# Kernel optimization log

Hardware: AMD Instinct MI355X
Metric: run time of the kernel (lower is better)

Reference implementation:

```python
import jax, jax.numpy as jnp
import numpy as np

NHEAD = 8
TOPKS = (8, 8)  # topk per level, coarse -> fine


def _to_bshd(x):
    # [B, C, H, W] -> [B, H*W, nhead, d]  (matches rearrange 'b c h w -> b (h w) c' + view)
    b, c, h, w = x.shape
    return jnp.transpose(x.reshape(b, c, h * w), (0, 2, 1)).reshape(b, h * w, NHEAD, c // NHEAD)


def _coarse_level(q, k, v, topk):
    b, c, h, w = k.shape
    d = c // NHEAD
    q_, k_, v_ = _to_bshd(q), _to_bshd(k), _to_bshd(v)
    temp = 1.0 / (d ** 0.5)
    A = jax.nn.softmax(jnp.einsum('nlhd,nshd->nlsh', q_, k_) * temp, axis=2)  # [b,L,S,h]
    _, idx = jax.lax.top_k(jnp.swapaxes(A, 2, 3), topk)  # [b,L,h,k]
    idx = jnp.swapaxes(idx, 2, 3)                        # [b,L,k,h]
    msg = jnp.einsum('nlsh,nshd->nlhd', A, v_)           # [b,L,h,d]
    topk_pos = jnp.stack([idx // w, idx % w])            # [2,b,L,k,h]
    return msg, topk_pos


def _fine_level(q, k, v, topk_pos, topk_prev, topk):
    b, c, h0, w0 = q.shape
    w1 = k.shape[3]
    d = c // NHEAD
    k_, v_ = _to_bshd(k), _to_bshd(v)
    H2, W2 = h0 // 2, w0 // 2
    L0 = H2 * W2
    # query grouped into 2x2 quads: [b, L0, 4, h, d]
    q_ = q.reshape(b, c, H2, 2, W2, 2).transpose(0, 2, 4, 3, 5, 1).reshape(b, L0, 4, NHEAD, d)
    tp = topk_pos * 2  # coarse positions -> fine grid
    cand = [(tp[0] + x) * w1 + tp[1] + y for x in (0, 1) for y in (0, 1)]
    t2 = topk_prev * 4
    idx = jnp.stack(cand, axis=3).reshape(b, L0, t2, NHEAD)  # [b,L,t2,h]
    idx_bh = idx.transpose(0, 3, 1, 2).reshape(b, NHEAD, L0 * t2)

    def gather(p):  # p: [b,S,h,d] -> gathered [b,L,t2,h,d]
        g = jnp.take_along_axis(jnp.swapaxes(p, 1, 2), idx_bh[..., None], axis=2)
        return g.reshape(b, NHEAD, L0, t2, d).transpose(0, 2, 3, 1, 4)

    tk, tv = gather(k_), gather(v_)
    temp = 1.0 / (d ** 0.5)
    A = jax.nn.softmax(jnp.einsum('blqhd,blthd->blqth', q_, tk) * temp, axis=3)  # [b,L,4,t2,h]
    _, ti = jax.lax.top_k(jnp.moveaxis(A, 3, 4), topk)  # [b,L,4,h,k]
    ti = jnp.moveaxis(ti, 4, 3)                         # [b,L,4,k,h]
    msg = jnp.einsum('blqth,blthd->blqhd', A, tv)       # [b,L,4,h,d]
    idx_b = jnp.broadcast_to(idx[:, :, None], (b, L0, 4, t2, NHEAD))
    gidx = jnp.take_along_axis(idx_b, ti, axis=3)       # [b,L,4,k,h] flat fine-grid indices
    gidx = gidx.reshape(b, H2, W2, 2, 2, topk, NHEAD).transpose(0, 1, 3, 2, 4, 5, 6)
    gidx = gidx.reshape(b, h0 * w0, topk, NHEAD)
    return msg, gidx


def _forward(q_fine, q_coarse, k_fine, k_coarse, v_fine, v_coarse, weight):
    msg0, topk_pos = _coarse_level(q_coarse, k_coarse, v_coarse, TOPKS[0])
    msg1, _ = _fine_level(q_fine, k_fine, v_fine, topk_pos, TOPKS[0], TOPKS[1])
    w = jax.nn.softmax(weight, axis=0)
    fm = msg0 * w[0]                  # [b,Lc,h,d]
    fm = fm[:, :, None] + msg1 * w[1]  # [b,Lc,4,h,d]
    b, Hc, Wc = q_coarse.shape[0], q_coarse.shape[2], q_coarse.shape[3]
    d = fm.shape[-1]
    # rearrange 'b (H W) (t1 t2) h d -> b (H t1 W t2) h d'
    fm = fm.reshape(b, Hc, Wc, 2, 2, NHEAD, d).transpose(0, 1, 3, 2, 4, 5, 6)
    return fm.reshape(b, Hc * Wc * 4, NHEAD, d)


def setup_inputs() -> dict:
    key = jax.random.key(0)
    ks = jax.random.split(key, 7)
    B, C = 4, 128
    return {
        'q_fine': jax.random.normal(ks[0], (B, C, 64, 64), jnp.float32),
        'q_coarse': jax.random.normal(ks[1], (B, C, 32, 32), jnp.float32),
        'k_fine': jax.random.normal(ks[2], (B, C, 64, 64), jnp.float32),
        'k_coarse': jax.random.normal(ks[3], (B, C, 32, 32), jnp.float32),
        'v_fine': jax.random.normal(ks[4], (B, C, 64, 64), jnp.float32),
        'v_coarse': jax.random.normal(ks[5], (B, C, 32, 32), jnp.float32),
        'weight': jax.random.normal(ks[6], (2,), jnp.float32),
    }


def reference(q_fine, q_coarse, k_fine, k_coarse, v_fine, v_coarse, weight):
    return _forward(q_fine, q_coarse, k_fine, k_coarse, v_fine, v_coarse, weight)
```

## Files before the change

kernel.cpp:

```cpp
#include <hip/hip_runtime.h>
#include <stdint.h>

#define TEMP 0.25f

typedef unsigned short u16;
typedef short v8s __attribute__((ext_vector_type(8)));
typedef float v4f __attribute__((ext_vector_type(4)));

static __device__ __forceinline__ uint32_t f2b_bits(float f){
    union { float f; uint32_t i; } x; x.f = f;
    uint32_t u = x.i;
    return (u + 0x7FFFu + ((u >> 16) & 1u)) >> 16;
}
static __device__ __forceinline__ float b2f(u16 u){
    union { uint32_t i; float f; } x; x.i = ((uint32_t)u) << 16; return x.f;
}
static __device__ __forceinline__ float bl(uint32_t u){
    union { uint32_t i; float f; } x; x.i = u << 16; return x.f;
}
static __device__ __forceinline__ float bh(uint32_t u){
    union { uint32_t i; float f; } x; x.i = u & 0xffff0000u; return x.f;
}
static __device__ __forceinline__ uint4 pack8(const uint32_t* e){
    return make_uint4(e[0] | (e[1] << 16), e[2] | (e[3] << 16),
                      e[4] | (e[5] << 16), e[6] | (e[7] << 16));
}
static __device__ __forceinline__ uint32_t split2_pk(float x){
    float hi = __uint_as_float(__float_as_uint(x) & 0xffff0000u);
    float lo = x - hi;
    uint32_t pk;
    asm("v_cvt_pk_bf16_f32 %0, %1, %2" : "=v"(pk) : "v"(hi), "v"(lo));
    return pk;
}
union U8S { uint4 u; v8s s; };
union I4S { int i[4]; v8s s; };
static __device__ __forceinline__ v8s asv8s(uint4 u){ U8S x; x.u = u; return x.s; }

template<int C>
static __device__ __forceinline__ float dppf(float x){
    int xi = __float_as_int(x);
    return __int_as_float(__builtin_amdgcn_update_dpp(xi, xi, C, 0xf, 0xf, false));
}
static __device__ __forceinline__ float red16_max(float m){
    m = fmaxf(m, dppf<0xB1>(m));  m = fmaxf(m, dppf<0x4E>(m));
    m = fmaxf(m, dppf<0x141>(m)); m = fmaxf(m, dppf<0x140>(m));
    return m;
}
static __device__ __forceinline__ float red16_sum(float s){
    s += dppf<0xB1>(s);  s += dppf<0x4E>(s);
    s += dppf<0x141>(s); s += dppf<0x140>(s);
    return s;
}
static __device__ __forceinline__ float sw16(float x){
    return __int_as_float(__builtin_amdgcn_ds_swizzle(__float_as_int(x), 0x401F));
}
template<int C>
static __device__ __forceinline__ uint64_t dppmax64(uint64_t k){
    int hi = (int)(uint32_t)(k >> 32), lo = (int)(uint32_t)k;
    uint32_t oh = (uint32_t)__builtin_amdgcn_update_dpp(hi, hi, C, 0xf, 0xf, false);
    uint32_t ol = (uint32_t)__builtin_amdgcn_update_dpp(lo, lo, C, 0xf, 0xf, false);
    uint64_t ok = ((uint64_t)oh << 32) | ol;
    return ok > k ? ok : k;
}
static __device__ __forceinline__ uint64_t red16_maxkey(uint64_t k){
    k = dppmax64<0xB1>(k);  k = dppmax64<0x4E>(k);
    k = dppmax64<0x141>(k); k = dppmax64<0x140>(k);
    return k;
}

__global__ __launch_bounds__(256)
void pack_coarse(const float* __restrict__ kc, const float* __restrict__ vc,
                 uint4* __restrict__ KP1, uint4* __restrict__ KP3,
                 uint4* __restrict__ VP1)
{
    const int bh = blockIdx.x;
    const int kv = blockIdx.y;
    const int z  = blockIdx.z;
    const int b = bh >> 3, h = bh & 7;
    const int tid = threadIdx.x;
    const size_t sbase = (size_t)(b * 128 + h * 16) * 1024;
    const size_t fbase = (size_t)bh * 64 * 64;

    #pragma unroll
    for (int it = 0; it < 2; ++it){
        int task = it * 256 + tid;
        int kt = z * 8 + (task >> 6), ln = task & 63;
        int quad = ln >> 4, col = ln & 15;
        if (kv == 0){
            uint32_t e1[8], e3[8];
            #pragma unroll
            for (int j = 0; j < 8; ++j){
                int dch = (quad & 1) * 8 + j;
                float x = kc[sbase + (size_t)dch * 1024 + kt * 16 + col];
                uint32_t u0 = f2b_bits(x);
                float r1 = x - b2f((u16)u0);
                uint32_t u1 = f2b_bits(r1);
                float r2 = r1 - b2f((u16)u1);
                uint32_t u2 = f2b_bits(r2);
                e1[j] = (quad < 2) ? u0 : u1;
                e3[j] = (quad < 2) ? u2 : u0;
            }
            KP1[fbase + kt * 64 + ln] = pack8(e1);
            KP3[fbase + kt * 64 + ln] = pack8(e3);
        } else {
            uint32_t e[8];
            #pragma unroll
            for (int j = 0; j < 8; ++j){
                int key = kt * 16 + (quad & 1) * 8 + j;
                float x = vc[sbase + (size_t)col * 1024 + key];
                uint32_t u0 = f2b_bits(x);
                uint32_t u1 = f2b_bits(x - b2f((u16)u0));
                e[j] = (quad < 2) ? u0 : u1;
            }
            VP1[fbase + kt * 64 + ln] = pack8(e);
        }
    }
}

__global__ __launch_bounds__(256)
void pack_all(const float* __restrict__ kf, const float* __restrict__ vf,
              const float* __restrict__ qf,
              const float* __restrict__ kc, const float* __restrict__ vc,
              uint32_t* __restrict__ packed, float* __restrict__ qT,
              uint4* __restrict__ KP1, uint4* __restrict__ KP3,
              uint4* __restrict__ VP1)
{
    __shared__ float tile[64][129];
    const int bid = blockIdx.x;
    const int tid = threadIdx.x;

    if (bid < 768){
        const int pt = bid & 63, b = (bid >> 6) & 3, z = bid >> 8;
        const float* src = (z == 0) ? kf : (z == 1) ? vf : qf;
        const int pos0 = pt * 64;

        #pragma unroll
        for (int it = 0; it < 8; ++it){
            int task = it * 256 + tid;
            int ch = task >> 4, p4 = task & 15;
            float4 v = *(const float4*)(src + (size_t)(b * 128 + ch) * 4096 + pos0 + p4 * 4);
            tile[p4*4+0][ch] = v.x; tile[p4*4+1][ch] = v.y;
            tile[p4*4+2][ch] = v.z; tile[p4*4+3][ch] = v.w;
        }
        __syncthreads();

        if (z == 2){
            #pragma unroll
            for (int it = 0; it < 8; ++it){
                int task = it * 256 + tid;
                int p = task >> 5, c4 = task & 31;
                float4 v = make_float4(tile[p][c4*4+0], tile[p][c4*4+1],
                                       tile[p][c4*4+2], tile[p][c4*4+3]);
                *(float4*)(qT + ((size_t)(b * 4096) + pos0 + p) * 128 + c4 * 4) = v;
            }
        } else {
            const int x = pt;
            #pragma unroll
            for (int it = 0; it < 2; ++it){
                int task = it * 256 + tid;
                int hq = task >> 6, y = task & 63;
                int pprime = ((x >> 1) * 32 + (y >> 1)) * 4 + (x & 1) * 2 + (y & 1);
                size_t line = (size_t)(b * 8 + hq) * 4096 + pprime;
                uint32_t dw[8];
                #pragma unroll
                for (int i = 0; i < 8; ++i){
                    uint32_t lo = f2b_bits(tile[y][hq * 16 + 2 * i]);
                    uint32_t hi = f2b_bits(tile[y][hq * 16 + 2 * i + 1]);
                    dw[i] = lo | (hi << 16);
                }
                uint4* dst4 = (uint4*)packed + line * 4 + z * 2;
                dst4[0] = make_uint4(dw[0], dw[1], dw[2], dw[3]);
                dst4[1] = make_uint4(dw[4], dw[5], dw[6], dw[7]);
            }
        }
    } else {
        const int f2 = bid - 768;
        const int bh = f2 & 31, kv = (f2 >> 5) & 1, z = f2 >> 6;
        const int b = bh >> 3, h = bh & 7;
        const size_t sbase = (size_t)(b * 128 + h * 16) * 1024;
        const size_t fbase = (size_t)bh * 64 * 64;

        #pragma unroll
        for (int it = 0; it < 2; ++it){
            int task = it * 256 + tid;
            int kt = z * 8 + (task >> 6), ln = task & 63;
            int quad = ln >> 4, col = ln & 15;
            if (kv == 0){
                uint32_t e1[8], e3[8];
                #pragma unroll
                for (int j = 0; j < 8; ++j){
                    int dch = (quad & 1) * 8 + j;
                    float x = kc[sbase + (size_t)dch * 1024 + kt * 16 + col];
                    uint32_t u0 = f2b_bits(x);
                    float r1 = x - b2f((u16)u0);
                    uint32_t u1 = f2b_bits(r1);
                    float r2 = r1 - b2f((u16)u1);
                    uint32_t u2 = f2b_bits(r2);
                    e1[j] = (quad < 2) ? u0 : u1;
                    e3[j] = (quad < 2) ? u2 : u0;
                }
                KP1[fbase + kt * 64 + ln] = pack8(e1);
                KP3[fbase + kt * 64 + ln] = pack8(e3);
            } else {
                uint32_t e[8];
                #pragma unroll
                for (int j = 0; j < 8; ++j){
                    int key = kt * 16 + (quad & 1) * 8 + j;
                    float x = vc[sbase + (size_t)col * 1024 + key];
                    uint32_t pk = split2_pk(x);
                    e[j] = (quad < 2) ? (pk & 0xffffu) : (pk >> 16);
                }
                VP1[fbase + kt * 64 + ln] = pack8(e);
            }
        }
    }
}

__global__ __launch_bounds__(256)
void coarse_mfma(const float* __restrict__ qc,
                 const uint4* __restrict__ KP1, const uint4* __restrict__ KP3,
                 const uint4* __restrict__ VP1,
                 float* __restrict__ msg0, int* __restrict__ topk_out)
{
    const int ltile = blockIdx.x;
    const int h = blockIdx.y, b = blockIdx.z;
    const int bh = b * 8 + h;
    const int tid = threadIdx.x, lane = tid & 63, wv = tid >> 6;
    const int quad = lane >> 4, col = lane & 15;
    const int lanex = lane ^ 32;
    const int lbase = ltile * 16;

    __shared__ uint32_t tls[4][2 * 320];
    __shared__ float rred[2][4][16];
    __shared__ float pvred[4][16][16];
    __shared__ float tkv[4][16][8];
    __shared__ int   tki[4][16][8];

    v8s a1, a3;
    {
        int row = lbase + col;
        int dch0 = (quad & 1) * 8;
        #pragma unroll
        for (int j = 0; j < 8; ++j){
            float x = qc[(size_t)(b * 128 + h * 16 + dch0 + j) * 1024 + row] * TEMP;
            uint32_t u0 = f2b_bits(x);
            float r1 = x - b2f((u16)u0);
            uint32_t u1 = f2b_bits(r1);
            float r2 = r1 - b2f((u16)u1);
            uint32_t u2 = f2b_bits(r2);
            a1[j] = (short)(quad < 2 ? u0 : u1);
            a3[j] = (short)(quad < 2 ? u0 : u2);
        }
    }

    const size_t fbase = (size_t)bh * 64 * 64;
    v4f sc[16];
    #pragma unroll
    for (int kt = 0; kt < 16; ++kt){
        int ktg = wv * 16 + kt;
        v8s b1 = asv8s(KP1[fbase + (size_t)ktg * 64 + lane]);
        v8s b2 = asv8s(KP1[fbase + (size_t)ktg * 64 + lanex]);
        v8s b3 = asv8s(KP3[fbase + (size_t)ktg * 64 + lane]);
        v4f c = {0.f, 0.f, 0.f, 0.f};
        c = __builtin_amdgcn_mfma_f32_16x16x32_bf16(a1, b1, c, 0, 0, 0);
        c = __builtin_amdgcn_mfma_f32_16x16x32_bf16(a1, b2, c, 0, 0, 0);
        c = __builtin_amdgcn_mfma_f32_16x16x32_bf16(a3, b3, c, 0, 0, 0);
        sc[kt] = c;
    }

    #pragma unroll
    for (int r = 0; r < 4; ++r){
        float m = sc[0][r];
        #pragma unroll
        for (int kt = 1; kt < 16; ++kt) m = fmaxf(m, sc[kt][r]);
        m = red16_max(m);
        if (col == 0) rred[0][wv][quad * 4 + r] = m;
    }
    __syncthreads();
    #pragma unroll
    for (int r = 0; r < 4; ++r){
        int row = quad * 4 + r;
        float m = fmaxf(fmaxf(rred[0][0][row], rred[0][1][row]),
                        fmaxf(rred[0][2][row], rred[0][3][row]));
        #pragma unroll
        for (int kt = 0; kt < 16; ++kt) sc[kt][r] = __expf(sc[kt][r] - m);
    }
    #pragma unroll
    for (int r = 0; r < 4; ++r){
        float s = 0.f;
        #pragma unroll
        for (int kt = 0; kt < 16; ++kt) s += sc[kt][r];
        s = red16_sum(s);
        if (col == 0) rred[1][wv][quad * 4 + r] = s;
    }

    v4f acc = {0.f, 0.f, 0.f, 0.f};
    uint32_t* tw = tls[wv];
    const int rdbase = col * 20 + 8 * (quad & 1);
    const uint32_t selp = (quad < 2) ? 0x05040100u : 0x07060302u;
    #pragma unroll
    for (int kb = 0; kb < 8; ++kb){
        #pragma unroll
        for (int ki = 0; ki < 2; ++ki){
            int kt = kb * 2 + ki;
            #pragma unroll
            for (int r = 0; r < 4; ++r)
                tw[ki * 320 + (quad * 4 + r) * 20 + col] = split2_pk(sc[kt][r]);
        }
        __builtin_amdgcn_s_waitcnt(0xC07F);
        #pragma unroll
        for (int ki = 0; ki < 2; ++ki){
            int kt = kb * 2 + ki;
            uint4 d0 = *(const uint4*)&tw[ki * 320 + rdbase];
            uint4 d1 = *(const uint4*)&tw[ki * 320 + rdbase + 4];
            I4S ux;
            ux.i[0] = __builtin_amdgcn_perm(d0.y, d0.x, selp);
            ux.i[1] = __builtin_amdgcn_perm(d0.w, d0.z, selp);
            ux.i[2] = __builtin_amdgcn_perm(d1.y, d1.x, selp);
            ux.i[3] = __builtin_amdgcn_perm(d1.w, d1.z, selp);
            v8s ap = ux.s;
            v8s bv1 = asv8s(VP1[fbase + (size_t)(wv * 16 + kt) * 64 + lane]);
            v8s bv2 = asv8s(VP1[fbase + (size_t)(wv * 16 + kt) * 64 + lanex]);
            acc = __builtin_amdgcn_mfma_f32_16x16x32_bf16(ap, bv1, acc, 0, 0, 0);
            acc = __builtin_amdgcn_mfma_f32_16x16x32_bf16(ap, bv2, acc, 0, 0, 0);
        }
    }
    #pragma unroll
    for (int r = 0; r < 4; ++r) pvred[wv][quad * 4 + r][col] = acc[r];

    #pragma unroll
    for (int r = 0; r < 4; ++r){
        int row = quad * 4 + r;
        float wval = 0.f; int widx = 0;
        #pragma unroll
        for (int rnd = 0; rnd < 8; ++rnd){
            float bv = sc[0][r]; int bk = 0;
            #pragma unroll
            for (int kt = 1; kt < 16; ++kt){
                bool g = sc[kt][r] > bv;
                bv = g ? sc[kt][r] : bv; bk = g ? kt : bk;
            }
            int bi = bk * 16 + col;
            uint64_t k = ((uint64_t)(uint32_t)__float_as_int(bv) << 32)
                       | (uint32_t)(~bi);
            k = red16_maxkey(k);
            bv = __int_as_float((int)(uint32_t)(k >> 32));
            bi = (int)(~(uint32_t)k);
            if ((bi & 15) == col){
                int ktw = bi >> 4;
                #pragma unroll
                for (int kt = 0; kt < 16; ++kt)
                    if (kt == ktw) sc[kt][r] = -1.0f;
            }
            if (col == rnd){ wval = bv; widx = wv * 256 + bi; }
        }
        if (col < 8){ tkv[wv][row][col] = wval; tki[wv][row][col] = widx; }
    }
    __syncthreads();

    {
        int row = tid >> 4, dd = tid & 15;
        float v = pvred[0][row][dd] + pvred[1][row][dd] +
                  pvred[2][row][dd] + pvred[3][row][dd];
        float s = rred[1][0][row] + rred[1][1][row] +
                  rred[1][2][row] + rred[1][3][row];
        msg0[((size_t)((b * 1024 + lbase + row) * 8 + h)) * 16 + dd] = v / s;
    }
    if (tid < 16){
        int row = tid;
        int* tp = topk_out + (((b * 1024 + lbase + row) * 8 + h) * 8);
        int p[4] = {0, 0, 0, 0};
        #pragma unroll
        for (int rnd = 0; rnd < 8; ++rnd){
            float bv = -3.0f; int bw = 0, bi = 0x7fffffff;
            #pragma unroll
            for (int w = 0; w < 4; ++w){
                float v = tkv[w][row][p[w]];
                int   i = tki[w][row][p[w]];
                bool g = (v > bv) || (v == bv && i < bi);
                bv = g ? v : bv; bi = g ? i : bi; bw = g ? w : bw;
            }
            tp[rnd] = bi;
            p[bw]++;
        }
    }
}

__global__ __launch_bounds__(512, 2)
void coarse_kernel(const float* __restrict__ qc, const float* __restrict__ kc,
                   const float* __restrict__ vc, float* __restrict__ msg0,
                   int* __restrict__ topk_out)
{
    const int ltile = blockIdx.x;
    const int h = blockIdx.y, b = blockIdx.z;
    const int tid = threadIdx.x;
    const int lane = tid & 63, wv = tid >> 6;
    const int lbase = ltile * 32;
    __shared__ float sKV[16 * 1024];
    const size_t base = (size_t)(b * 128 + h * 16) * 1024;
    {
        const float4* gK = (const float4*)(kc + base);
        float4* lK = (float4*)sKV;
        #pragma unroll
        for (int i = 0; i < 8; ++i) lK[tid + 512 * i] = gK[tid + 512 * i];
    }
    float qreg[4];
    {
        int dq = lane & 15;
        #pragma unroll
        for (int li = 0; li < 4; ++li){
            int l = lbase + wv * 4 + li;
            qreg[li] = qc[base + (size_t)dq * 1024 + l] * TEMP;
        }
    }
    __syncthreads();
    float p[4][16];
    #pragma unroll
    for (int li = 0; li < 4; ++li)
        #pragma unroll
        for (int j = 0; j < 16; ++j) p[li][j] = 0.f;
    #pragma unroll
    for (int dch = 0; dch < 16; ++dch){
        float kf[16];
        #pragma unroll
        for (int ch = 0; ch < 4; ++ch){
            float4 kv = *(const float4*)&sKV[dch * 1024 + ch * 256 + (lane << 2)];
            kf[ch*4+0] = kv.x; kf[ch*4+1] = kv.y; kf[ch*4+2] = kv.z; kf[ch*4+3] = kv.w;
        }
        float qs[4];
        #pragma unroll
        for (int li = 0; li < 4; ++li) qs[li] = __shfl(qreg[li], dch);
        #pragma unroll
        for (int li = 0; li < 4; ++li)
            #pragma unroll
            for (int j = 0; j < 16; ++j) p[li][j] = fmaf(qs[li], kf[j], p[li][j]);
    }
    float invs[4];
    #pragma unroll
    for (int li = 0; li < 4; ++li){
        float m = p[li][0];
        #pragma unroll
        for (int j = 1; j < 16; ++j) m = fmaxf(m, p[li][j]);
        #pragma unroll
        for (int off = 32; off > 0; off >>= 1) m = fmaxf(m, __shfl_xor(m, off));
        float s = 0.f;
        #pragma unroll
        for (int j = 0; j < 16; ++j){ p[li][j] = __expf(p[li][j] - m); s += p[li][j]; }
        #pragma unroll
        for (int off = 32; off > 0; off >>= 1) s += __shfl_xor(s, off);
        invs[li] = 1.0f / s;
    }
    __syncthreads();
    {
        const float4* gV = (const float4*)(vc + base);
        float4* lV = (float4*)sKV;
        #pragma unroll
        for (int i = 0; i < 8; ++i) lV[tid + 512 * i] = gV[tid + 512 * i];
    }
    __syncthreads();
    float outv = 0.f;
    #pragma unroll
    for (int dd = 0; dd < 16; ++dd){
        float vf[16];
        #pragma unroll
        for (int ch = 0; ch < 4; ++ch){
            float4 vv = *(const float4*)&sKV[dd * 1024 + ch * 256 + (lane << 2)];
            vf[ch*4+0] = vv.x; vf[ch*4+1] = vv.y; vf[ch*4+2] = vv.z; vf[ch*4+3] = vv.w;
        }
        float a[4];
        #pragma unroll
        for (int li = 0; li < 4; ++li){
            float s = 0.f;
            #pragma unroll
            for (int j = 0; j < 16; ++j) s = fmaf(p[li][j], vf[j], s);
            a[li] = s;
        }
        #pragma unroll
        for (int off = 32; off > 0; off >>= 1)
            #pragma unroll
            for (int li = 0; li < 4; ++li) a[li] += __shfl_xor(a[li], off);
        #pragma unroll
        for (int li = 0; li < 4; ++li)
            outv = (lane == li * 16 + dd) ? a[li] * invs[li] : outv;
    }
    {
        int li = lane >> 4, dd = lane & 15;
        int l = lbase + wv * 4 + li;
        msg0[(size_t)((b * 1024 + l) * 8 + h) * 16 + dd] = outv;
    }
    const int lanebase = lane << 4;
    int mytk = 0;
    for (int r = 0; r < 8; ++r){
        float bv[4]; int bi[4];
        #pragma unroll
        for (int li = 0; li < 4; ++li){
            float v0[8]; int j0[8];
            #pragma unroll
            for (int k = 0; k < 8; ++k){
                bool g = p[li][2*k+1] > p[li][2*k];
                v0[k] = g ? p[li][2*k+1] : p[li][2*k];
                j0[k] = g ? 2*k+1 : 2*k;
            }
            float v1[4]; int j1[4];
            #pragma unroll
            for (int k = 0; k < 4; ++k){
                bool g = v0[2*k+1] > v0[2*k];
                v1[k] = g ? v0[2*k+1] : v0[2*k];
                j1[k] = g ? j0[2*k+1] : j0[2*k];
            }
            float v2[2]; int j2[2];
            #pragma unroll
            for (int k = 0; k < 2; ++k){
                bool g = v1[2*k+1] > v1[2*k];
                v2[k] = g ? v1[2*k+1] : v1[2*k];
                j2[k] = g ? j1[2*k+1] : j1[2*k];
            }
            bool g3 = v2[1] > v2[0];
            bv[li] = g3 ? v2[1] : v2[0];
            bi[li] = lanebase | (g3 ? j2[1] : j2[0]);
        }
        #pragma unroll
        for (int off = 32; off > 0; off >>= 1){
            #pragma unroll
            for (int li = 0; li < 4; ++li){
                float ov = __shfl_xor(bv[li], off);
                int   oi = __shfl_xor(bi[li], off);
                bool g = (ov > bv[li]) || (ov == bv[li] && oi < bi[li]);
                bv[li] = g ? ov : bv[li];
                bi[li] = g ? oi : bi[li];
            }
        }
        #pragma unroll
        for (int li = 0; li < 4; ++li){
            #pragma unroll
            for (int j = 0; j < 16; ++j)
                p[li][j] = (bi[li] == (lanebase | j)) ? -1.0f : p[li][j];
            mytk = (lane == li * 8 + r) ? bi[li] : mytk;
        }
    }
    if (lane < 32){
        int li = lane >> 3, r = lane & 7;
        int jw = mytk & 15, lw = mytk >> 4;
        int s = ((jw >> 2) << 8) | (lw << 2) | (jw & 3);
        int l = lbase + wv * 4 + li;
        topk_out[((b * 1024 + l) * 8 + h) * 8 + r] = s;
    }
}

__global__ __launch_bounds__(256)
void pack_kernel(const float* __restrict__ kf, const float* __restrict__ vf,
                 const float* __restrict__ qf,
                 uint32_t* __restrict__ packed, float* __restrict__ qT)
{
    const int pt = blockIdx.x;
    const int b  = blockIdx.y;
    const int z  = blockIdx.z;
    const float* src = (z == 0) ? kf : (z == 1) ? vf : qf;
    const int tid = threadIdx.x;
    __shared__ float tile[64][129];
    const int pos0 = pt * 64;

    #pragma unroll
    for (int it = 0; it < 8; ++it){
        int task = it * 256 + tid;
        int ch = task >> 4, p4 = task & 15;
        float4 v = *(const float4*)(src + (size_t)(b * 128 + ch) * 4096 + pos0 + p4 * 4);
        tile[p4*4+0][ch] = v.x; tile[p4*4+1][ch] = v.y;
        tile[p4*4+2][ch] = v.z; tile[p4*4+3][ch] = v.w;
    }
    __syncthreads();

    if (z == 2){
        #pragma unroll
        for (int it = 0; it < 8; ++it){
            int task = it * 256 + tid;
            int p = task >> 5, c4 = task & 31;
            float4 v = make_float4(tile[p][c4*4+0], tile[p][c4*4+1],
                                   tile[p][c4*4+2], tile[p][c4*4+3]);
            *(float4*)(qT + ((size_t)(b * 4096) + pos0 + p) * 128 + c4 * 4) = v;
        }
    } else {
        const int x = pt;
        #pragma unroll
        for (int it = 0; it < 2; ++it){
            int task = it * 256 + tid;
            int h = task >> 6, y = task & 63;
            int pprime = ((x >> 1) * 32 + (y >> 1)) * 4 + (x & 1) * 2 + (y & 1);
            size_t line = (size_t)(b * 8 + h) * 4096 + pprime;
            uint32_t dw[8];
            #pragma unroll
            for (int i = 0; i < 8; ++i){
                uint32_t lo = f2b_bits(tile[y][h * 16 + 2 * i]);
                uint32_t hi = f2b_bits(tile[y][h * 16 + 2 * i + 1]);
                dw[i] = lo | (hi << 16);
            }
            uint4* dst4 = (uint4*)packed + line * 4 + z * 2;
            dst4[0] = make_uint4(dw[0], dw[1], dw[2], dw[3]);
            dst4[1] = make_uint4(dw[4], dw[5], dw[6], dw[7]);
        }
    }
}

__global__ __launch_bounds__(256)
void fine_kernel(const float* __restrict__ qf, const float* __restrict__ kf,
                 const float* __restrict__ vf,
                 const float* __restrict__ qTg, const uint32_t* __restrict__ packed,
                 int transposed,
                 const float* __restrict__ wt,
                 const int* __restrict__ topk_in, const float* __restrict__ msg0,
                 float* __restrict__ out)
{
    const int l0 = blockIdx.x;
    const int b  = blockIdx.y;
    const int tid = threadIdx.x;

    __shared__ float vT[8][16][34];
    __shared__ float qT[8][4][16];
    __shared__ float pT[8][4][32];
    __shared__ int tkS[8][8];

    if (tid < 64) tkS[tid >> 3][tid & 7] =
        topk_in[((b * 1024 + l0) * 8 + (tid >> 3)) * 8 + (tid & 7)];
    __syncthreads();

    const int i = l0 >> 5, j = l0 & 31;
    const int hh = tid >> 5;
    const int t  = tid & 31;
    const int kk = t >> 2, cp = t & 3;

    float k[16];
    {
        int s = tkS[hh][kk];
        if (transposed){
            const uint4* pk = (const uint4*)packed;
            size_t line = (size_t)(b * 8 + hh) * 4096 + s * 4 + cp;
            uint4 a0 = pk[line*4+0], a1 = pk[line*4+1];
            uint4 a2 = pk[line*4+2], a3 = pk[line*4+3];
            k[0]=bl(a0.x);  k[1]=bh(a0.x);  k[2]=bl(a0.y);  k[3]=bh(a0.y);
            k[4]=bl(a0.z);  k[5]=bh(a0.z);  k[6]=bl(a0.w);  k[7]=bh(a0.w);
            k[8]=bl(a1.x);  k[9]=bh(a1.x);  k[10]=bl(a1.y); k[11]=bh(a1.y);
            k[12]=bl(a1.z); k[13]=bh(a1.z); k[14]=bl(a1.w); k[15]=bh(a1.w);
            vT[hh][0][t]=bl(a2.x);  vT[hh][1][t]=bh(a2.x);
            vT[hh][2][t]=bl(a2.y);  vT[hh][3][t]=bh(a2.y);
            vT[hh][4][t]=bl(a2.z);  vT[hh][5][t]=bh(a2.z);
            vT[hh][6][t]=bl(a2.w);  vT[hh][7][t]=bh(a2.w);
            vT[hh][8][t]=bl(a3.x);  vT[hh][9][t]=bh(a3.x);
            vT[hh][10][t]=bl(a3.y); vT[hh][11][t]=bh(a3.y);
            vT[hh][12][t]=bl(a3.z); vT[hh][13][t]=bh(a3.z);
            vT[hh][14][t]=bl(a3.w); vT[hh][15][t]=bh(a3.w);
        } else {
            int pos = (2 * (s >> 5) + (cp >> 1)) * 64 + 2 * (s & 31) + (cp & 1);
            size_t gb = (size_t)(b * 128 + hh * 16) * 4096 + pos;
            #pragma unroll
            for (int ch = 0; ch < 16; ++ch){
                k[ch] = kf[gb + (size_t)ch * 4096];
                vT[hh][ch][t] = vf[gb + (size_t)ch * 4096];
            }
        }
    }
    if (tid < 128){
        int qh = tid >> 4, aq = (tid >> 2) & 3, c4 = tid & 3;
        int qpos = (2 * i + (aq >> 1)) * 64 + 2 * j + (aq & 1);
        if (transposed){
            float4 u = *(const float4*)(qTg + ((size_t)(b * 4096) + qpos) * 128 + qh * 16 + c4 * 4);
            qT[qh][aq][c4*4+0] = u.x * TEMP;
            qT[qh][aq][c4*4+1] = u.y * TEMP;
            qT[qh][aq][c4*4+2] = u.z * TEMP;
            qT[qh][aq][c4*4+3] = u.w * TEMP;
        } else {
            #pragma unroll
            for (int c = 0; c < 4; ++c)
                qT[qh][aq][c4*4+c] =
                    qf[(size_t)(b * 128 + qh * 16 + c4 * 4 + c) * 4096 + qpos] * TEMP;
        }
    }
    __syncthreads();

    {
        float sc[4] = {0.f, 0.f, 0.f, 0.f};
        #pragma unroll
        for (int dch = 0; dch < 16; ++dch){
            float kv = k[dch];
            #pragma unroll
            for (int q = 0; q < 4; ++q) sc[q] = fmaf(qT[hh][q][dch], kv, sc[q]);
        }
        #pragma unroll
        for (int q = 0; q < 4; ++q){
            float m = red16_max(sc[q]);
            m = fmaxf(m, sw16(m));
            float e = __expf(sc[q] - m);
            float s = red16_sum(e);
            s += sw16(s);
            pT[hh][q][t] = e / s;
        }
    }
    __syncthreads();

    {
        float w0 = wt[0], w1 = wt[1];
        float mx = fmaxf(w0, w1);
        float e0 = __expf(w0 - mx), e1 = __expf(w1 - mx);
        float w0f = e0 / (e0 + e1), w1f = e1 / (e0 + e1);

        int q0 = (tid >> 4) & 1;
        int dd = tid & 15;
        float a0 = 0.f, a1 = 0.f;
        #pragma unroll
        for (int tt = 0; tt < 16; ++tt){
            float v0 = vT[hh][dd][tt * 2], v1 = vT[hh][dd][tt * 2 + 1];
            float2 pA = *(const float2*)&pT[hh][q0][tt * 2];
            float2 pB = *(const float2*)&pT[hh][q0 + 2][tt * 2];
            a0 = fmaf(pA.x, v0, a0); a0 = fmaf(pA.y, v1, a0);
            a1 = fmaf(pB.x, v0, a1); a1 = fmaf(pB.y, v1, a1);
        }
        float m0 = msg0[(size_t)((b * 1024 + l0) * 8 + hh) * 16 + dd];
        float o0 = w0f * m0 + w1f * a0;
        float o1 = w0f * m0 + w1f * a1;
        int posA = (2 * i) * 64 + 2 * j + q0;
        int posB = (2 * i + 1) * 64 + 2 * j + q0;
        out[(size_t)((b * 4096 + posA) * 8 + hh) * 16 + dd] = o0;
        out[(size_t)((b * 4096 + posB) * 8 + hh) * 16 + dd] = o1;
    }
}

extern "C" void kernel_launch(void* const* d_in, const int* in_sizes, int n_in,
                              void* d_out, int out_size, void* d_ws, size_t ws_size,
                              hipStream_t stream)
{
    (void)in_sizes; (void)n_in; (void)out_size;

    const float* q_fine   = (const float*)d_in[0];
    const float* q_coarse = (const float*)d_in[1];
    const float* k_fine   = (const float*)d_in[2];
    const float* k_coarse = (const float*)d_in[3];
    const float* v_fine   = (const float*)d_in[4];
    const float* v_coarse = (const float*)d_in[5];
    const float* weight   = (const float*)d_in[6];

    const size_t MB = 1024 * 1024;
    float*    msg0   = (float*)d_ws;
    int*      topk   = (int*)((char*)d_ws + 2 * MB);
    float*    qT     = (float*)((char*)d_ws + 3 * MB);
    uint32_t* packed = (uint32_t*)((char*)d_ws + 11 * MB);
    uint4*    KP1    = (uint4*)((char*)d_ws + 19 * MB);
    uint4*    KP3    = (uint4*)((char*)d_ws + 21 * MB);
    uint4*    VP1    = (uint4*)((char*)d_ws + 23 * MB);
    const int doT = (ws_size >= 19 * MB) ? 1 : 0;
    const int doM = (ws_size >= 25 * MB) ? 1 : 0;

    if (doM && doT){
        pack_all<<<dim3(1280), dim3(256), 0, stream>>>(k_fine, v_fine, q_fine,
                                                       k_coarse, v_coarse,
                                                       packed, qT, KP1, KP3, VP1);
        coarse_mfma<<<dim3(64, 8, 4), dim3(256), 0, stream>>>(q_coarse, KP1, KP3, VP1,
                                                              msg0, topk);
    } else {
        if (doM){
            pack_coarse<<<dim3(32, 2, 8), dim3(256), 0, stream>>>(k_coarse, v_coarse,
                                                                  KP1, KP3, VP1);
            coarse_mfma<<<dim3(64, 8, 4), dim3(256), 0, stream>>>(q_coarse, KP1, KP3, VP1,
                                                                  msg0, topk);
        } else {
            coarse_kernel<<<dim3(32, 8, 4), dim3(512), 0, stream>>>(q_coarse, k_coarse,
                                                                    v_coarse, msg0, topk);
        }
        if (doT){
            pack_kernel<<<dim3(64, 4, 3), dim3(256), 0, stream>>>(k_fine, v_fine, q_fine,
                                                                  packed, qT);
        }
    }

    fine_kernel<<<dim3(1024, 4), dim3(256), 0, stream>>>(q_fine, k_fine, v_fine,
                                                         qT, packed, doT,
                                                         weight, topk, msg0,
                                                         (float*)d_out);
}
```

Baseline: 191.0 us.

## Fuse fine-level packing into coarse attention kernel and pack V as bf16 pairs

The fine K/V/Q transpose-and-pack work moves out of pack_all into extra blocks of a new coarse_fused kernel. That kernel shares a union shared-memory buffer, uses a smaller half-channel tile, and sets a launch-bounds occupancy hint. Coarse K/V packing now runs as its own small pack_coarse launch first. In the fine kernel, V is staged in shared memory as packed bf16 pairs instead of float, which halves LDS footprint and write count. The aim is to overlap packing with coarse MFMA work and raise occupancy, at the cost of one extra launch and a more branchy mixed kernel.

Result: slower. 321.7 us (+68.4%).

```diff
diff --git a/kernel.cpp b/kernel.cpp
--- a/kernel.cpp
+++ b/kernel.cpp
@@ -108,133 +108,97 @@
             for (int j = 0; j < 8; ++j){
                 int key = kt * 16 + (quad & 1) * 8 + j;
                 float x = vc[sbase + (size_t)col * 1024 + key];
-                uint32_t u0 = f2b_bits(x);
-                uint32_t u1 = f2b_bits(x - b2f((u16)u0));
-                e[j] = (quad < 2) ? u0 : u1;
+                uint32_t pk = split2_pk(x);
+                e[j] = (quad < 2) ? (pk & 0xffffu) : (pk >> 16);
             }
             VP1[fbase + kt * 64 + ln] = pack8(e);
         }
     }
 }
 
-__global__ __launch_bounds__(256)
-void pack_all(const float* __restrict__ kf, const float* __restrict__ vf,
-              const float* __restrict__ qf,
-              const float* __restrict__ kc, const float* __restrict__ vc,
-              uint32_t* __restrict__ packed, float* __restrict__ qT,
-              uint4* __restrict__ KP1, uint4* __restrict__ KP3,
-              uint4* __restrict__ VP1)
+struct CoarseSM {
+    uint32_t tls[4][640];
+    float rred[2][4][16];
+    float pvred[4][16][16];
+    float tkv[4][16][8];
+    int   tki[4][16][8];
+};
+union FusedSM {
+    CoarseSM c;
+    float tile[64][65];
+};
+
+__global__ __launch_bounds__(256, 6)
+void coarse_fused(const float* __restrict__ qc,
+                  const uint4* __restrict__ KP1, const uint4* __restrict__ KP3,
+                  const uint4* __restrict__ VP1,
+                  float* __restrict__ msg0, int* __restrict__ topk_out,
+                  const float* __restrict__ kf, const float* __restrict__ vf,
+                  const float* __restrict__ qf,
+                  uint32_t* __restrict__ packed, float* __restrict__ qT)
 {
-    __shared__ float tile[64][129];
+    __shared__ FusedSM sm;
     const int bid = blockIdx.x;
     const int tid = threadIdx.x;
 
-    if (bid < 768){
-        const int pt = bid & 63, b = (bid >> 6) & 3, z = bid >> 8;
+    if (bid >= 2048){
+        const int pid = bid - 2048;
+        const int pt = pid & 63, b = (pid >> 6) & 3, z = pid >> 8;
         const float* src = (z == 0) ? kf : (z == 1) ? vf : qf;
         const int pos0 = pt * 64;
 
         #pragma unroll
-        for (int it = 0; it < 8; ++it){
-            int task = it * 256 + tid;
-            int ch = task >> 4, p4 = task & 15;
-            float4 v = *(const float4*)(src + (size_t)(b * 128 + ch) * 4096 + pos0 + p4 * 4);
-            tile[p4*4+0][ch] = v.x; tile[p4*4+1][ch] = v.y;
-            tile[p4*4+2][ch] = v.z; tile[p4*4+3][ch] = v.w;
-        }
-        __syncthreads();
-
-        if (z == 2){
-            #pragma unroll
-            for (int it = 0; it < 8; ++it){
+        for (int half = 0; half < 2; ++half){
+            #pragma unroll
+            for (int it = 0; it < 4; ++it){
                 int task = it * 256 + tid;
-                int p = task >> 5, c4 = task & 31;
-                float4 v = make_float4(tile[p][c4*4+0], tile[p][c4*4+1],
-                                       tile[p][c4*4+2], tile[p][c4*4+3]);
-                *(float4*)(qT + ((size_t)(b * 4096) + pos0 + p) * 128 + c4 * 4) = v;
-            }
-        } else {
-            const int x = pt;
-            #pragma unroll
-            for (int it = 0; it < 2; ++it){
-                int task = it * 256 + tid;
-                int hq = task >> 6, y = task & 63;
-                int pprime = ((x >> 1) * 32 + (y >> 1)) * 4 + (x & 1) * 2 + (y & 1);
+                int ch = task >> 4, p4 = task & 15;
+                float4 v = *(const float4*)(src +
+                    (size_t)(b * 128 + half * 64 + ch) * 4096 + pos0 + p4 * 4);
+                sm.tile[p4*4+0][ch] = v.x; sm.tile[p4*4+1][ch] = v.y;
+                sm.tile[p4*4+2][ch] = v.z; sm.tile[p4*4+3][ch] = v.w;
+            }
+            __syncthreads();
+
+            if (z == 2){
+                #pragma unroll
+                for (int it = 0; it < 4; ++it){
+                    int task = it * 256 + tid;
+                    int p = task >> 4, c4 = task & 15;
+                    float4 v = make_float4(sm.tile[p][c4*4+0], sm.tile[p][c4*4+1],
+                                           sm.tile[p][c4*4+2], sm.tile[p][c4*4+3]);
+                    *(float4*)(qT + ((size_t)(b * 4096) + pos0 + p) * 128
+                                  + half * 64 + c4 * 4) = v;
+                }
+            } else {
+                int hq = half * 4 + (tid >> 6), y = tid & 63;
+                int hql = tid >> 6;
+                int pprime = ((pt >> 1) * 32 + (y >> 1)) * 4 + (pt & 1) * 2 + (y & 1);
                 size_t line = (size_t)(b * 8 + hq) * 4096 + pprime;
                 uint32_t dw[8];
                 #pragma unroll
                 for (int i = 0; i < 8; ++i){
-                    uint32_t lo = f2b_bits(tile[y][hq * 16 + 2 * i]);
-                    uint32_t hi = f2b_bits(tile[y][hq * 16 + 2 * i + 1]);
+                    uint32_t lo = f2b_bits(sm.tile[y][hql * 16 + 2 * i]);
+                    uint32_t hi = f2b_bits(sm.tile[y][hql * 16 + 2 * i + 1]);
                     dw[i] = lo | (hi << 16);
                 }
                 uint4* dst4 = (uint4*)packed + line * 4 + z * 2;
                 dst4[0] = make_uint4(dw[0], dw[1], dw[2], dw[3]);
                 dst4[1] = make_uint4(dw[4], dw[5], dw[6], dw[7]);
             }
-        }
-    } else {
-        const int f2 = bid - 768;
-        const int bh = f2 & 31, kv = (f2 >> 5) & 1, z = f2 >> 6;
-        const int b = bh >> 3, h = bh & 7;
-        const size_t sbase = (size_t)(b * 128 + h * 16) * 1024;
-        const size_t fbase = (size_t)bh * 64 * 64;
-
-        #pragma unroll
-        for (int it = 0; it < 2; ++it){
-            int task = it * 256 + tid;
-            int kt = z * 8 + (task >> 6), ln = task & 63;
-            int quad = ln >> 4, col = ln & 15;
-            if (kv == 0){
-                uint32_t e1[8], e3[8];
-                #pragma unroll
-                for (int j = 0; j < 8; ++j){
-                    int dch = (quad & 1) * 8 + j;
-                    float x = kc[sbase + (size_t)dch * 1024 + kt * 16 + col];
-                    uint32_t u0 = f2b_bits(x);
-                    float r1 = x - b2f((u16)u0);
-                    uint32_t u1 = f2b_bits(r1);
-                    float r2 = r1 - b2f((u16)u1);
-                    uint32_t u2 = f2b_bits(r2);
-                    e1[j] = (quad < 2) ? u0 : u1;
-                    e3[j] = (quad < 2) ? u2 : u0;
-                }
-                KP1[fbase + kt * 64 + ln] = pack8(e1);
-                KP3[fbase + kt * 64 + ln] = pack8(e3);
-            } else {
-                uint32_t e[8];
-                #pragma unroll
-                for (int j = 0; j < 8; ++j){
-                    int key = kt * 16 + (quad & 1) * 8 + j;
-                    float x = vc[sbase + (size_t)col * 1024 + key];
-                    uint32_t pk = split2_pk(x);
-                    e[j] = (quad < 2) ? (pk & 0xffffu) : (pk >> 16);
-                }
-                VP1[fbase + kt * 64 + ln] = pack8(e);
-            }
-        }
-    }
-}
-
-__global__ __launch_bounds__(256)
-void coarse_mfma(const float* __restrict__ qc,
-                 const uint4* __restrict__ KP1, const uint4* __restrict__ KP3,
-                 const uint4* __restrict__ VP1,
-                 float* __restrict__ msg0, int* __restrict__ topk_out)
-{
-    const int ltile = blockIdx.x;
-    const int h = blockIdx.y, b = blockIdx.z;
+            __syncthreads();
+        }
+        return;
+    }
+
+    const int ltile = bid & 63;
+    const int h = (bid >> 6) & 7, b = bid >> 9;
     const int bh = b * 8 + h;
-    const int tid = threadIdx.x, lane = tid & 63, wv = tid >> 6;
+    const int lane = tid & 63, wv = tid >> 6;
     const int quad = lane >> 4, col = lane & 15;
     const int lanex = lane ^ 32;
     const int lbase = ltile * 16;
-
-    __shared__ uint32_t tls[4][2 * 320];
-    __shared__ float rred[2][4][16];
-    __shared__ float pvred[4][16][16];
-    __shared__ float tkv[4][16][8];
-    __shared__ int   tki[4][16][8];
+    CoarseSM& C = sm.c;
 
     v8s a1, a3;
     {
@@ -274,14 +238,14 @@
         #pragma unroll
         for (int kt = 1; kt < 16; ++kt) m = fmaxf(m, sc[kt][r]);
         m = red16_max(m);
-        if (col == 0) rred[0][wv][quad * 4 + r] = m;
+        if (col == 0) C.rred[0][wv][quad * 4 + r] = m;
     }
     __syncthreads();
     #pragma unroll
     for (int r = 0; r < 4; ++r){
         int row = quad * 4 + r;
-        float m = fmaxf(fmaxf(rred[0][0][row], rred[0][1][row]),
-                        fmaxf(rred[0][2][row], rred[0][3][row]));
+        float m = fmaxf(fmaxf(C.rred[0][0][row], C.rred[0][1][row]),
+                        fmaxf(C.rred[0][2][row], C.rred[0][3][row]));
         #pragma unroll
         for (int kt = 0; kt < 16; ++kt) sc[kt][r] = __expf(sc[kt][r] - m);
     }
@@ -291,11 +255,11 @@
         #pragma unroll
         for (int kt = 0; kt < 16; ++kt) s += sc[kt][r];
         s = red16_sum(s);
-        if (col == 0) rred[1][wv][quad * 4 + r] = s;
+        if (col == 0) C.rred[1][wv][quad * 4 + r] = s;
     }
 
     v4f acc = {0.f, 0.f, 0.f, 0.f};
-    uint32_t* tw = tls[wv];
+    uint32_t* tw = C.tls[wv];
     const int rdbase = col * 20 + 8 * (quad & 1);
     const uint32_t selp = (quad < 2) ? 0x05040100u : 0x07060302u;
     #pragma unroll
@@ -326,7 +290,7 @@
         }
     }
     #pragma unroll
-    for (int r = 0; r < 4; ++r) pvred[wv][quad * 4 + r][col] = acc[r];
+    for (int r = 0; r < 4; ++r) C.pvred[wv][quad * 4 + r][col] = acc[r];
 
     #pragma unroll
     for (int r = 0; r < 4; ++r){
@@ -354,16 +318,16 @@
             }
             if (col == rnd){ wval = bv; widx = wv * 256 + bi; }
         }
-        if (col < 8){ tkv[wv][row][col] = wval; tki[wv][row][col] = widx; }
+        if (col < 8){ C.tkv[wv][row][col] = wval; C.tki[wv][row][col] = widx; }
     }
     __syncthreads();
 
     {
         int row = tid >> 4, dd = tid & 15;
-        float v = pvred[0][row][dd] + pvred[1][row][dd] +
-                  pvred[2][row][dd] + pvred[3][row][dd];
-        float s = rred[1][0][row] + rred[1][1][row] +
-                  rred[1][2][row] + rred[1][3][row];
+        float v = C.pvred[0][row][dd] + C.pvred[1][row][dd] +
+                  C.pvred[2][row][dd] + C.pvred[3][row][dd];
+        float s = C.rred[1][0][row] + C.rred[1][1][row] +
+                  C.rred[1][2][row] + C.rred[1][3][row];
         msg0[((size_t)((b * 1024 + lbase + row) * 8 + h)) * 16 + dd] = v / s;
     }
     if (tid < 16){
@@ -375,8 +339,174 @@
             float bv = -3.0f; int bw = 0, bi = 0x7fffffff;
             #pragma unroll
             for (int w = 0; w < 4; ++w){
-                float v = tkv[w][row][p[w]];
-                int   i = tki[w][row][p[w]];
+                float v = C.tkv[w][row][p[w]];
+                int   i = C.tki[w][row][p[w]];
+                bool g = (v > bv) || (v == bv && i < bi);
+                bv = g ? v : bv; bi = g ? i : bi; bw = g ? w : bw;
+            }
+            tp[rnd] = bi;
+            p[bw]++;
+        }
+    }
+}
+
+__global__ __launch_bounds__(256)
+void coarse_mfma(const float* __restrict__ qc,
+                 const uint4* __restrict__ KP1, const uint4* __restrict__ KP3,
+                 const uint4* __restrict__ VP1,
+                 float* __restrict__ msg0, int* __restrict__ topk_out)
+{
+    const int ltile = blockIdx.x;
+    const int h = blockIdx.y, b = blockIdx.z;
+    const int bh = b * 8 + h;
+    const int tid = threadIdx.x, lane = tid & 63, wv = tid >> 6;
+    const int quad = lane >> 4, col = lane & 15;
+    const int lanex = lane ^ 32;
+    const int lbase = ltile * 16;
+
+    __shared__ CoarseSM C;
+
+    v8s a1, a3;
+    {
+        int row = lbase + col;
+        int dch0 = (quad & 1) * 8;
+        #pragma unroll
+        for (int j = 0; j < 8; ++j){
+            float x = qc[(size_t)(b * 128 + h * 16 + dch0 + j) * 1024 + row] * TEMP;
+            uint32_t u0 = f2b_bits(x);
+            float r1 = x - b2f((u16)u0);
+            uint32_t u1 = f2b_bits(r1);
+            float r2 = r1 - b2f((u16)u1);
+            uint32_t u2 = f2b_bits(r2);
+            a1[j] = (short)(quad < 2 ? u0 : u1);
+            a3[j] = (short)(quad < 2 ? u0 : u2);
+        }
+    }
+
+    const size_t fbase = (size_t)bh * 64 * 64;
+    v4f sc[16];
+    #pragma unroll
+    for (int kt = 0; kt < 16; ++kt){
+        int ktg = wv * 16 + kt;
+        v8s b1 = asv8s(KP1[fbase + (size_t)ktg * 64 + lane]);
+        v8s b2 = asv8s(KP1[fbase + (size_t)ktg * 64 + lanex]);
+        v8s b3 = asv8s(KP3[fbase + (size_t)ktg * 64 + lane]);
+        v4f c = {0.f, 0.f, 0.f, 0.f};
+        c = __builtin_amdgcn_mfma_f32_16x16x32_bf16(a1, b1, c, 0, 0, 0);
+        c = __builtin_amdgcn_mfma_f32_16x16x32_bf16(a1, b2, c, 0, 0, 0);
+        c = __builtin_amdgcn_mfma_f32_16x16x32_bf16(a3, b3, c, 0, 0, 0);
+        sc[kt] = c;
+    }
+
+    #pragma unroll
+    for (int r = 0; r < 4; ++r){
+        float m = sc[0][r];
+        #pragma unroll
+        for (int kt = 1; kt < 16; ++kt) m = fmaxf(m, sc[kt][r]);
+        m = red16_max(m);
+        if (col == 0) C.rred[0][wv][quad * 4 + r] = m;
+    }
+    __syncthreads();
+    #pragma unroll
+    for (int r = 0; r < 4; ++r){
+        int row = quad * 4 + r;
+        float m = fmaxf(fmaxf(C.rred[0][0][row], C.rred[0][1][row]),
+                        fmaxf(C.rred[0][2][row], C.rred[0][3][row]));
+        #pragma unroll
+        for (int kt = 0; kt < 16; ++kt) sc[kt][r] = __expf(sc[kt][r] - m);
+    }
+    #pragma unroll
+    for (int r = 0; r < 4; ++r){
+        float s = 0.f;
+        #pragma unroll
+        for (int kt = 0; kt < 16; ++kt) s += sc[kt][r];
+        s = red16_sum(s);
+        if (col == 0) C.rred[1][wv][quad * 4 + r] = s;
+    }
+
+    v4f acc = {0.f, 0.f, 0.f, 0.f};
+    uint32_t* tw = C.tls[wv];
+    const int rdbase = col * 20 + 8 * (quad & 1);
+    const uint32_t selp = (quad < 2) ? 0x05040100u : 0x07060302u;
+    #pragma unroll
+    for (int kb = 0; kb < 8; ++kb){
+        #pragma unroll
+        for (int ki = 0; ki < 2; ++ki){
+            int kt = kb * 2 + ki;
+            #pragma unroll
+            for (int r = 0; r < 4; ++r)
+                tw[ki * 320 + (quad * 4 + r) * 20 + col] = split2_pk(sc[kt][r]);
+        }
+        __builtin_amdgcn_s_waitcnt(0xC07F);
+        #pragma unroll
+        for (int ki = 0; ki < 2; ++ki){
+            int kt = kb * 2 + ki;
+            uint4 d0 = *(const uint4*)&tw[ki * 320 + rdbase];
+            uint4 d1 = *(const uint4*)&tw[ki * 320 + rdbase + 4];
+            I4S ux;
+            ux.i[0] = __builtin_amdgcn_perm(d0.y, d0.x, selp);
+            ux.i[1] = __builtin_amdgcn_perm(d0.w, d0.z, selp);
+            ux.i[2] = __builtin_amdgcn_perm(d1.y, d1.x, selp);
+            ux.i[3] = __builtin_amdgcn_perm(d1.w, d1.z, selp);
+            v8s ap = ux.s;
+            v8s bv1 = asv8s(VP1[fbase + (size_t)(wv * 16 + kt) * 64 + lane]);
+            v8s bv2 = asv8s(VP1[fbase + (size_t)(wv * 16 + kt) * 64 + lanex]);
+            acc = __builtin_amdgcn_mfma_f32_16x16x32_bf16(ap, bv1, acc, 0, 0, 0);
+            acc = __builtin_amdgcn_mfma_f32_16x16x32_bf16(ap, bv2, acc, 0, 0, 0);
+        }
+    }
+    #pragma unroll
+    for (int r = 0; r < 4; ++r) C.pvred[wv][quad * 4 + r][col] = acc[r];
+
+    #pragma unroll
+    for (int r = 0; r < 4; ++r){
+        int row = quad * 4 + r;
+        float wval = 0.f; int widx = 0;
+        #pragma unroll
+        for (int rnd = 0; rnd < 8; ++rnd){
+            float bv = sc[0][r]; int bk = 0;
+            #pragma unroll
+            for (int kt = 1; kt < 16; ++kt){
+                bool g = sc[kt][r] > bv;
+                bv = g ? sc[kt][r] : bv; bk = g ? kt : bk;
+            }
+            int bi = bk * 16 + col;
+            uint64_t k = ((uint64_t)(uint32_t)__float_as_int(bv) << 32)
+                       | (uint32_t)(~bi);
+            k = red16_maxkey(k);
+            bv = __int_as_float((int)(uint32_t)(k >> 32));
+            bi = (int)(~(uint32_t)k);
+            if ((bi & 15) == col){
+                int ktw = bi >> 4;
+                #pragma unroll
+                for (int kt = 0; kt < 16; ++kt)
+                    if (kt == ktw) sc[kt][r] = -1.0f;
+            }
+            if (col == rnd){ wval = bv; widx = wv * 256 + bi; }
+        }
+        if (col < 8){ C.tkv[wv][row][col] = wval; C.tki[wv][row][col] = widx; }
+    }
+    __syncthreads();
+
+    {
+        int row = tid >> 4, dd = tid & 15;
+        float v = C.pvred[0][row][dd] + C.pvred[1][row][dd] +
+                  C.pvred[2][row][dd] + C.pvred[3][row][dd];
+        float s = C.rred[1][0][row] + C.rred[1][1][row] +
+                  C.rred[1][2][row] + C.rred[1][3][row];
+        msg0[((size_t)((b * 1024 + lbase + row) * 8 + h)) * 16 + dd] = v / s;
+    }
+    if (tid < 16){
+        int row = tid;
+        int* tp = topk_out + (((b * 1024 + lbase + row) * 8 + h) * 8);
+        int p[4] = {0, 0, 0, 0};
+        #pragma unroll
+        for (int rnd = 0; rnd < 8; ++rnd){
+            float bv = -3.0f; int bw = 0, bi = 0x7fffffff;
+            #pragma unroll
+            for (int w = 0; w < 4; ++w){
+                float v = C.tkv[w][row][p[w]];
+                int   i = C.tki[w][row][p[w]];
                 bool g = (v > bv) || (v == bv && i < bi);
                 bv = g ? v : bv; bi = g ? i : bi; bw = g ? w : bw;
             }
@@ -421,11 +551,11 @@
         for (int j = 0; j < 16; ++j) p[li][j] = 0.f;
     #pragma unroll
     for (int dch = 0; dch < 16; ++dch){
-        float kf[16];
+        float kfv[16];
         #pragma unroll
         for (int ch = 0; ch < 4; ++ch){
             float4 kv = *(const float4*)&sKV[dch * 1024 + ch * 256 + (lane << 2)];
-            kf[ch*4+0] = kv.x; kf[ch*4+1] = kv.y; kf[ch*4+2] = kv.z; kf[ch*4+3] = kv.w;
+            kfv[ch*4+0] = kv.x; kfv[ch*4+1] = kv.y; kfv[ch*4+2] = kv.z; kfv[ch*4+3] = kv.w;
         }
         float qs[4];
         #pragma unroll
@@ -433,7 +563,7 @@
         #pragma unroll
         for (int li = 0; li < 4; ++li)
             #pragma unroll
-            for (int j = 0; j < 16; ++j) p[li][j] = fmaf(qs[li], kf[j], p[li][j]);
+            for (int j = 0; j < 16; ++j) p[li][j] = fmaf(qs[li], kfv[j], p[li][j]);
     }
     float invs[4];
     #pragma unroll
@@ -461,18 +591,18 @@
     float outv = 0.f;
     #pragma unroll
     for (int dd = 0; dd < 16; ++dd){
-        float vf[16];
+        float vf2[16];
         #pragma unroll
         for (int ch = 0; ch < 4; ++ch){
             float4 vv = *(const float4*)&sKV[dd * 1024 + ch * 256 + (lane << 2)];
-            vf[ch*4+0] = vv.x; vf[ch*4+1] = vv.y; vf[ch*4+2] = vv.z; vf[ch*4+3] = vv.w;
+            vf2[ch*4+0] = vv.x; vf2[ch*4+1] = vv.y; vf2[ch*4+2] = vv.z; vf2[ch*4+3] = vv.w;
         }
         float a[4];
         #pragma unroll
         for (int li = 0; li < 4; ++li){
             float s = 0.f;
             #pragma unroll
-            for (int j = 0; j < 16; ++j) s = fmaf(p[li][j], vf[j], s);
+            for (int j = 0; j < 16; ++j) s = fmaf(p[li][j], vf2[j], s);
             a[li] = s;
         }
         #pragma unroll
@@ -614,7 +744,7 @@
     const int b  = blockIdx.y;
     const int tid = threadIdx.x;
 
-    __shared__ float vT[8][16][34];
+    __shared__ uint32_t vTp[8][8][33];
     __shared__ float qT[8][4][16];
     __shared__ float pT[8][4][32];
     __shared__ int tkS[8][8];
@@ -640,21 +770,22 @@
             k[4]=bl(a0.z);  k[5]=bh(a0.z);  k[6]=bl(a0.w);  k[7]=bh(a0.w);
             k[8]=bl(a1.x);  k[9]=bh(a1.x);  k[10]=bl(a1.y); k[11]=bh(a1.y);
             k[12]=bl(a1.z); k[13]=bh(a1.z); k[14]=bl(a1.w); k[15]=bh(a1.w);
-            vT[hh][0][t]=bl(a2.x);  vT[hh][1][t]=bh(a2.x);
-            vT[hh][2][t]=bl(a2.y);  vT[hh][3][t]=bh(a2.y);
-            vT[hh][4][t]=bl(a2.z);  vT[hh][5][t]=bh(a2.z);
-            vT[hh][6][t]=bl(a2.w);  vT[hh][7][t]=bh(a2.w);
-            vT[hh][8][t]=bl(a3.x);  vT[hh][9][t]=bh(a3.x);
-            vT[hh][10][t]=bl(a3.y); vT[hh][11][t]=bh(a3.y);
-            vT[hh][12][t]=bl(a3.z); vT[hh][13][t]=bh(a3.z);
-            vT[hh][14][t]=bl(a3.w); vT[hh][15][t]=bh(a3.w);
+            vTp[hh][0][t] = a2.x; vTp[hh][1][t] = a2.y;
+            vTp[hh][2][t] = a2.z; vTp[hh][3][t] = a2.w;
+            vTp[hh][4][t] = a3.x; vTp[hh][5][t] = a3.y;
+            vTp[hh][6][t] = a3.z; vTp[hh][7][t] = a3.w;
         } else {
             int pos = (2 * (s >> 5) + (cp >> 1)) * 64 + 2 * (s & 31) + (cp & 1);
             size_t gb = (size_t)(b * 128 + hh * 16) * 4096 + pos;
             #pragma unroll
-            for (int ch = 0; ch < 16; ++ch){
-                k[ch] = kf[gb + (size_t)ch * 4096];
-                vT[hh][ch][t] = vf[gb + (size_t)ch * 4096];
+            for (int ch = 0; ch < 16; ++ch) k[ch] = kf[gb + (size_t)ch * 4096];
+            #pragma unroll
+            for (int c2 = 0; c2 < 8; ++c2){
+                float f0 = vf[gb + (size_t)(2 * c2) * 4096];
+                float f1 = vf[gb + (size_t)(2 * c2 + 1) * 4096];
+                uint32_t pkv;
+                asm("v_cvt_pk_bf16_f32 %0, %1, %2" : "=v"(pkv) : "v"(f0), "v"(f1));
+                vTp[hh][c2][t] = pkv;
             }
         }
     }
@@ -704,10 +835,15 @@
 
         int q0 = (tid >> 4) & 1;
         int dd = tid & 15;
+        int cpair = dd >> 1;
+        int sh = (dd & 1) << 4;
         float a0 = 0.f, a1 = 0.f;
         #pragma unroll
         for (int tt = 0; tt < 16; ++tt){
-            float v0 = vT[hh][dd][tt * 2], v1 = vT[hh][dd][tt * 2 + 1];
+            uint32_t u0 = vTp[hh][cpair][tt * 2];
+            uint32_t u1 = vTp[hh][cpair][tt * 2 + 1];
+            float v0 = __uint_as_float((u0 >> sh) << 16);
+            float v1 = __uint_as_float((u1 >> sh) << 16);
             float2 pA = *(const float2*)&pT[hh][q0][tt * 2];
             float2 pB = *(const float2*)&pT[hh][q0 + 2][tt * 2];
             a0 = fmaf(pA.x, v0, a0); a0 = fmaf(pA.y, v1, a0);
@@ -748,22 +884,20 @@
     const int doT = (ws_size >= 19 * MB) ? 1 : 0;
     const int doM = (ws_size >= 25 * MB) ? 1 : 0;
 
-    if (doM && doT){
-        pack_all<<<dim3(1280), dim3(256), 0, stream>>>(k_fine, v_fine, q_fine,
-                                                       k_coarse, v_coarse,
-                                                       packed, qT, KP1, KP3, VP1);
-        coarse_mfma<<<dim3(64, 8, 4), dim3(256), 0, stream>>>(q_coarse, KP1, KP3, VP1,
-                                                              msg0, topk);
+    if (doM){
+        pack_coarse<<<dim3(32, 2, 8), dim3(256), 0, stream>>>(k_coarse, v_coarse,
+                                                              KP1, KP3, VP1);
+        if (doT){
+            coarse_fused<<<dim3(2816), dim3(256), 0, stream>>>(
+                q_coarse, KP1, KP3, VP1, msg0, topk,
+                k_fine, v_fine, q_fine, packed, qT);
+        } else {
+            coarse_mfma<<<dim3(64, 8, 4), dim3(256), 0, stream>>>(q_coarse, KP1, KP3,
+                                                                  VP1, msg0, topk);
+        }
     } else {
-        if (doM){
-            pack_coarse<<<dim3(32, 2, 8), dim3(256), 0, stream>>>(k_coarse, v_coarse,
-                                                                  KP1, KP3, VP1);
-            coarse_mfma<<<dim3(64, 8, 4), dim3(256), 0, stream>>>(q_coarse, KP1, KP3, VP1,
-                                                                  msg0, topk);
-        } else {
-            coarse_kernel<<<dim3(32, 8, 4), dim3(512), 0, stream>>>(q_coarse, k_coarse,
-                                                                    v_coarse, msg0, topk);
-        }
+        coarse_kernel<<<dim3(32, 8, 4), dim3(512), 0, stream>>>(q_coarse, k_coarse,
+                                                                v_coarse, msg0, topk);
         if (doT){
             pack_kernel<<<dim3(64, 4, 3), dim3(256), 0, stream>>>(k_fine, v_fine, q_fine,
                                                                   packed, qT);
```
